# Kernel optimization log

Hardware: AMD Instinct MI355X
Metric: run time of the kernel (lower is better)

Reference implementation:

```python
import jax, jax.numpy as jnp
import numpy as np

B, S, HID = 2, 2048, 2048
H, HKV, HD = 16, 8, 128
INPUT_CHUNK, RET_CHUNK = 256, 64
NUM_CHUNKS = S // INPUT_CHUNK - 1          # 7 retrieval chunks
INPUT_START = NUM_CHUNKS * RET_CHUNK       # 448
KV_LEN = S + INPUT_START                   # 2496
SCALE = HD ** -0.5


def _document_id():
    d = np.zeros(KV_LEN, np.int32)
    d[INPUT_START:] = -1
    for i in range(NUM_CHUNKS):            # retrieval chunks get ids 1..NUM_CHUNKS
        d[RET_CHUNK * i: RET_CHUNK * (i + 1)] = i + 1
    for i in range(1, NUM_CHUNKS + 1):     # input chunk i (i>=1) gets id i
        d[INPUT_START + INPUT_CHUNK * i: INPUT_START + INPUT_CHUNK * (i + 1)] = i
    return d


def _causal_retrieval_mask():
    d = _document_id()
    q = np.arange(S)[:, None]
    kv = np.arange(KV_LEN)[None, :]
    causal = (q + INPUT_START >= kv) & (kv > INPUT_START)
    docm = (d[q + INPUT_START] == d[kv]) & (kv < INPUT_START)
    return jnp.asarray(causal | docm)      # [S, KV_LEN] bool


_MASK = _causal_retrieval_mask()


def rotate_half(x):
    x1, x2 = jnp.split(x, 2, axis=-1)
    return jnp.concatenate([-x2, x1], axis=-1)


def setup_inputs() -> dict:
    key = jax.random.key(0)
    ks = jax.random.split(key, 8)
    hidden_states = jax.random.normal(ks[0], (B, S, HID), jnp.float32)
    # standard llama RoPE tables
    pos = jnp.arange(S, dtype=jnp.float32)
    inv = 1.0 / (10000.0 ** (jnp.arange(0, HD, 2, dtype=jnp.float32) / HD))
    f = pos[:, None] * inv[None, :]
    emb = jnp.concatenate([f, f], axis=-1)
    cos = jnp.broadcast_to(jnp.cos(emb), (B, S, HD)).astype(jnp.float32)
    sin = jnp.broadcast_to(jnp.sin(emb), (B, S, HD)).astype(jnp.float32)
    retrieval_key_states = jax.random.normal(ks[1], (B * NUM_CHUNKS, HKV, RET_CHUNK, HD), jnp.float32)
    retrieval_value_states = jax.random.normal(ks[2], (B * NUM_CHUNKS, HKV, RET_CHUNK, HD), jnp.float32)
    s = 0.02
    Wq = jax.random.normal(ks[3], (HID, H * HD), jnp.float32) * s
    Wk = jax.random.normal(ks[4], (HID, HKV * HD), jnp.float32) * s
    Wv = jax.random.normal(ks[5], (HID, HKV * HD), jnp.float32) * s
    Wo = jax.random.normal(ks[6], (H * HD, HID), jnp.float32) * s
    return {"hidden_states": hidden_states, "cos": cos, "sin": sin,
            "retrieval_key_states": retrieval_key_states,
            "retrieval_value_states": retrieval_value_states,
            "Wq": Wq, "Wk": Wk, "Wv": Wv, "Wo": Wo}


def reference(hidden_states, cos, sin, retrieval_key_states, retrieval_value_states, Wq, Wk, Wv, Wo):
    b = hidden_states.shape[0]
    # QKV projections (bias=False), -> [b, h, s, d]
    q = (hidden_states @ Wq).reshape(b, S, H, HD).transpose(0, 2, 1, 3)
    k = (hidden_states @ Wk).reshape(b, S, HKV, HD).transpose(0, 2, 1, 3)
    v = (hidden_states @ Wv).reshape(b, S, HKV, HD).transpose(0, 2, 1, 3)
    # RoPE (cos/sin unsqueezed over heads)
    c = cos[:, None]
    sn = sin[:, None]
    q = q * c + rotate_half(q) * sn
    k = k * c + rotate_half(k) * sn
    # retrieval KV: (b*nc, hkv, rc, d) -> (b, hkv, nc*rc, d)
    rk = retrieval_key_states.reshape(b, NUM_CHUNKS, HKV, RET_CHUNK, HD).transpose(0, 2, 1, 3, 4).reshape(b, HKV, NUM_CHUNKS * RET_CHUNK, HD)
    rv = retrieval_value_states.reshape(b, NUM_CHUNKS, HKV, RET_CHUNK, HD).transpose(0, 2, 1, 3, 4).reshape(b, HKV, NUM_CHUNKS * RET_CHUNK, HD)
    k_all = jnp.concatenate([rk, k], axis=2)     # [b, hkv, KV_LEN, d]
    v_all = jnp.concatenate([rv, v], axis=2)
    # GQA: repeat kv heads
    g = H // HKV
    k_all = jnp.repeat(k_all, g, axis=1)
    v_all = jnp.repeat(v_all, g, axis=1)
    scores = jnp.einsum('bhqd,bhkd->bhqk', q, k_all) * SCALE
    neg = jnp.finfo(scores.dtype).min
    scores = jnp.where(_MASK[None, None], scores, neg)
    probs = jax.nn.softmax(scores, axis=-1)
    # fully-masked rows (q_idx=0) -> 0 output, matching flex_attention semantics
    probs = jnp.where(_MASK[None, None], probs, 0.0)
    attn = jnp.einsum('bhqk,bhkd->bhqd', probs, v_all)   # [b, H, S, HD]
    # NOTE: source reshapes (b, H, S, HD) directly to (b, S, H*HD) with NO transpose
    attn = attn.reshape(b, S, H * HD)
    return attn @ Wo
```

## Files before the change

### kernel.cpp

```cpp
#include <hip/hip_runtime.h>

#define B_ 2
#define S_ 2048
#define HID_ 2048
#define H_ 16
#define HKV_ 8
#define HD_ 128
#define NCH_ 7
#define RET_ 64
#define IST_ 448
#define KVL_ 2496
#define SCALE_ 0.08838834764831845f
#define SC2_ (0.08838834764831845f * 1.44269504088896340f)
#define MCAP_ 16.0f

typedef __attribute__((ext_vector_type(8))) short short8;
typedef __attribute__((ext_vector_type(4))) short short4v;
typedef __attribute__((ext_vector_type(4))) float f32x4;

static __device__ __forceinline__ unsigned short f2bf(float f) {
    unsigned u = __float_as_uint(f);
    unsigned r = (u + 0x7fffu + ((u >> 16) & 1u)) >> 16;
    return (unsigned short)r;
}
static __device__ __forceinline__ float bf2f(unsigned short x) {
    return __uint_as_float(((unsigned)x) << 16);
}

#define GLL16(gp, lp) __builtin_amdgcn_global_load_lds( \
    (__attribute__((address_space(1))) void*)(void*)(gp), \
    (__attribute__((address_space(3))) void*)(void*)(lp), 16, 0, 0)

__global__ __launch_bounds__(256) void prep_in_kernel(const float* __restrict__ hidden,
                                                      const float* __restrict__ Wq,
                                                      const float* __restrict__ Wk,
                                                      const float* __restrict__ Wv,
                                                      const float* __restrict__ Wo,
                                                      unsigned short* __restrict__ hb,
                                                      unsigned short* __restrict__ wqkvT,
                                                      unsigned short* __restrict__ woT) {
    const int bid = blockIdx.x;
    const int tid = threadIdx.x;
    if (bid < 8192) {
        int i = bid * 256 + tid;
        float4 v = ((const float4*)hidden)[i];
        ushort4 o;
        o.x = f2bf(v.x); o.y = f2bf(v.y); o.z = f2bf(v.z); o.w = f2bf(v.w);
        ((ushort4*)hb)[i] = o;
    } else {
        __shared__ float t[32][33];
        const int tbid = bid - 8192;
        const int z = tbid >> 12;
        const int xy = tbid & 4095;
        const int k0 = (xy & 63) << 5, n0 = (xy >> 6) << 5;
        const float* W;
        unsigned short* WT;
        int N;
        if (z == 0)      { W = Wq; WT = wqkvT;                        N = 2048; }
        else if (z == 1) { W = Wk; WT = wqkvT + (size_t)2048 * 2048;  N = 1024; }
        else if (z == 2) { W = Wv; WT = wqkvT + (size_t)3072 * 2048;  N = 1024; }
        else             { W = Wo; WT = woT;                          N = 2048; }
        if (n0 >= N) return;
        const int tx = tid & 31, ty = tid >> 5;
#pragma unroll
        for (int i = 0; i < 4; i++)
            t[ty + i * 8][tx] = W[(size_t)(k0 + ty + i * 8) * N + n0 + tx];
        __syncthreads();
#pragma unroll
        for (int i = 0; i < 4; i++)
            WT[(size_t)(n0 + ty + i * 8) * 2048 + k0 + tx] = f2bf(t[tx][ty + i * 8]);
    }
}

template <int BN, typename OT>
__global__ __launch_bounds__(512, 2) void gemm256(const unsigned short* __restrict__ A,
                                                  const unsigned short* __restrict__ BT,
                                                  OT* __restrict__ C,
                                                  int M, int N, int K) {
    constexpr int NJ = BN / 64;
    __shared__ short As[2][16384];
    __shared__ short Bs[2][BN * 64];
    const int tid = threadIdx.x;
    const int wid = tid >> 6, lane = tid & 63;
    const int lq = lane & 15, lk = lane >> 4;
    const int wm = wid >> 2, wn = wid & 3;
    const int bm = blockIdx.x, bn = blockIdx.y;

    const int rowin = tid >> 3;
    const int koff = (((tid & 7) ^ (rowin & 7)) << 3);
    const size_t abase = (size_t)(bm * 256 + rowin) * K;
    const size_t bbase = (size_t)(bn * BN + rowin) * K;
    const int ldst = wid * 512;

    f32x4 acc[8][NJ] = {};

    auto stageA = [&](int buf, int k0, int r) {
        GLL16(A + abase + (size_t)(r * 64) * K + k0 + koff, &As[buf][r * 4096 + ldst]);
    };
    auto stageB = [&](int buf, int k0, int r) {
        GLL16(BT + bbase + (size_t)(r * 64) * K + k0 + koff, &Bs[buf][r * 4096 + ldst]);
    };
    auto stageAll = [&](int buf, int k0) {
#pragma unroll
        for (int r = 0; r < 4; r++) stageA(buf, k0, r);
#pragma unroll
        for (int r = 0; r < NJ; r++) stageB(buf, k0, r);
    };

    const int nk = K >> 6;
    stageAll(0, 0);
    __syncthreads();
    for (int t = 0; t < nk; t++) {
        const int cur = t & 1;
        const bool pf = (t + 1 < nk);
        const int nk0 = (t + 1) << 6;
        short8 bf[2][NJ];
#pragma unroll
        for (int j = 0; j < NJ; j++)
#pragma unroll
            for (int kk = 0; kk < 2; kk++) {
                const int row = wn * (BN / 4) + j * 16 + lq;
                bf[kk][j] = *(const short8*)&Bs[cur][row * 64 +
                                                     (((kk * 4 + lk) ^ (lq & 7)) << 3)];
            }
#pragma unroll
        for (int p = 0; p < 4; p++) {
            if (pf) {
                stageA(cur ^ 1, nk0, p);
                if (p < NJ) stageB(cur ^ 1, nk0, p);
            }
            short8 af0[2], af1[2];
#pragma unroll
            for (int kk = 0; kk < 2; kk++) {
                const int r0 = wm * 128 + (2 * p) * 16 + lq;
                const int r1 = wm * 128 + (2 * p + 1) * 16 + lq;
                af0[kk] = *(const short8*)&As[cur][r0 * 64 +
                                                   (((kk * 4 + lk) ^ (lq & 7)) << 3)];
                af1[kk] = *(const short8*)&As[cur][r1 * 64 +
                                                   (((kk * 4 + lk) ^ (lq & 7)) << 3)];
            }
            __builtin_amdgcn_s_setprio(1);
#pragma unroll
            for (int j = 0; j < NJ; j++)
#pragma unroll
                for (int kk = 0; kk < 2; kk++) {
                    acc[2 * p][j] =
                        __builtin_amdgcn_mfma_f32_16x16x32_bf16(bf[kk][j], af0[kk], acc[2 * p][j], 0, 0, 0);
                    acc[2 * p + 1][j] =
                        __builtin_amdgcn_mfma_f32_16x16x32_bf16(bf[kk][j], af1[kk], acc[2 * p + 1][j], 0, 0, 0);
                }
            __builtin_amdgcn_s_setprio(0);
        }
        __syncthreads();
    }
#pragma unroll
    for (int i = 0; i < 8; i++) {
        const size_t row = (size_t)(bm * 256 + wm * 128 + i * 16 + lq);
#pragma unroll
        for (int j = 0; j < NJ; j++) {
            const size_t col = (size_t)(bn * BN + wn * (BN / 4) + j * 16 + lk * 4);
            if constexpr (sizeof(OT) == 2) {
                ushort4 u;
                u.x = f2bf(acc[i][j][0]);
                u.y = f2bf(acc[i][j][1]);
                u.z = f2bf(acc[i][j][2]);
                u.w = f2bf(acc[i][j][3]);
                *(ushort4*)&C[row * N + col] = u;
            } else {
                *(f32x4*)&C[row * N + col] = acc[i][j];
            }
        }
    }
}

__global__ __launch_bounds__(256) void prep_kv_kernel(const unsigned short* __restrict__ qkvraw,
                                                      const float* __restrict__ cosb,
                                                      const float* __restrict__ sinb,
                                                      const float* __restrict__ rk,
                                                      const float* __restrict__ rv,
                                                      unsigned short* __restrict__ kall,
                                                      unsigned short* __restrict__ vt) {
    const int bid = blockIdx.x;
    const int tid = threadIdx.x;
    if (bid < 2048) {
        unsigned u = (unsigned)bid * 256 + tid;
        int d0 = (u & 15) << 2;
        int hk = (u >> 4) & 7;
        unsigned bs = u >> 7;
        int b = (int)(bs >> 11), s = (int)(bs & 2047);
        size_t base = (size_t)bs * 4096 + 2048 + hk * 128 + d0;
        short4v x1 = *(const short4v*)(qkvraw + base);
        short4v x2 = *(const short4v*)(qkvraw + base + 64);
        float4 c1 = *(const float4*)(cosb + (size_t)s * 128 + d0);
        float4 s1 = *(const float4*)(sinb + (size_t)s * 128 + d0);
        float4 c2 = *(const float4*)(cosb + (size_t)s * 128 + d0 + 64);
        float4 s2 = *(const float4*)(sinb + (size_t)s * 128 + d0 + 64);
        const float cc1[4] = {c1.x, c1.y, c1.z, c1.w}, ss1[4] = {s1.x, s1.y, s1.z, s1.w};
        const float cc2[4] = {c2.x, c2.y, c2.z, c2.w}, ss2[4] = {s2.x, s2.y, s2.z, s2.w};
        size_t o = ((size_t)(b * HKV_ + hk) * KVL_ + IST_ + s) * HD_ + d0;
        ushort4 w1, w2;
        unsigned short r1[4], r2[4];
#pragma unroll
        for (int e = 0; e < 4; e++) {
            float a = bf2f((unsigned short)x1[e]);
            float bb = bf2f((unsigned short)x2[e]);
            r1[e] = f2bf(a * cc1[e] - bb * ss1[e]);
            r2[e] = f2bf(bb * cc2[e] + a * ss2[e]);
        }
        w1.x = r1[0]; w1.y = r1[1]; w1.z = r1[2]; w1.w = r1[3];
        w2.x = r2[0]; w2.y = r2[1]; w2.z = r2[2]; w2.w = r2[3];
        *(ushort4*)(kall + o) = w1;
        *(ushort4*)(kall + o + 64) = w2;
    } else if (bid < 2944) {
        unsigned u = (unsigned)(bid - 2048) * 256 + tid;
        int d0 = (u & 31) << 2;
        int r = (u >> 5) & 63;
        int hk = (u >> 11) & 7;
        int bc = (int)(u >> 14);
        int b = bc / NCH_, ch = bc % NCH_;
        float4 v = *(const float4*)(rk + (((size_t)(bc * HKV_ + hk) * RET_ + r) * HD_ + d0));
        ushort4 w;
        w.x = f2bf(v.x); w.y = f2bf(v.y); w.z = f2bf(v.z); w.w = f2bf(v.w);
        *(ushort4*)(kall + ((size_t)(b * HKV_ + hk) * KVL_ + ch * RET_ + r) * HD_ + d0) = w;
    } else {
        const int vbid = bid - 2944;
        const int tx = tid & 31, ty = tid >> 5;
        if (vbid < 4096) {
            __shared__ unsigned short t[32][33];
            const int d0 = (vbid & 3) << 5, s0 = ((vbid >> 2) & 63) << 5;
            const int bh = vbid >> 8;
            const int b = bh >> 3, hk = bh & 7;
#pragma unroll
            for (int i = 0; i < 4; i++)
                t[ty + i * 8][tx] =
                    qkvraw[(size_t)(b * S_ + s0 + ty + i * 8) * 4096 + 3072 + hk * 128 + d0 + tx];
            __syncthreads();
#pragma unroll
            for (int i = 0; i < 4; i++)
                vt[((size_t)(b * HKV_ + hk) * HD_ + d0 + ty + i * 8) * KVL_ + IST_ + s0 + tx] =
                    t[tx][ty + i * 8];
        } else {
            __shared__ float tf[32][33];
            const int bid2 = vbid - 4096;
            const int d0 = (bid2 & 3) << 5;
            const int r0 = ((bid2 >> 2) & 1) << 5;
            const int z = bid2 >> 3;
            const int bc = z >> 3, hk = z & 7;
            const int b = bc / NCH_, ch = bc % NCH_;
#pragma unroll
            for (int i = 0; i < 4; i++)
                tf[ty + i * 8][tx] =
                    rv[((size_t)(bc * HKV_ + hk) * RET_ + r0 + ty + i * 8) * HD_ + d0 + tx];
            __syncthreads();
#pragma unroll
            for (int i = 0; i < 4; i++)
                vt[((size_t)(b * HKV_ + hk) * HD_ + d0 + ty + i * 8) * KVL_ + ch * RET_ + r0 + tx] =
                    f2bf(tf[tx][ty + i * 8]);
        }
    }
}

__global__ __launch_bounds__(1024) void attn_kernel(const unsigned short* __restrict__ qkvraw,
                                                    const unsigned short* __restrict__ kall,
                                                    const unsigned short* __restrict__ vt,
                                                    const float* __restrict__ cosb,
                                                    const float* __restrict__ sinb,
                                                    unsigned short* __restrict__ attnb) {
    __shared__ short Ks[2][16384];
    __shared__ short Vs[2][16384];
    __shared__ short Ps[16][1024];
    const int tid = threadIdx.x;
    const int wid = tid >> 6, lane = tid & 63;
    const int lq = lane & 15, lk = lane >> 4;
    const int pairi = blockIdx.x;
    const int h = blockIdx.y, b = blockIdx.z, hk = h >> 1;
    const unsigned short* kbase = kall + (size_t)(b * HKV_ + hk) * KVL_ * HD_;
    const unsigned short* vbase = vt + (size_t)(b * HKV_ + hk) * HD_ * KVL_;

    int row_[2], xc_[2];
#pragma unroll
    for (int p = 0; p < 2; p++) {
        int o = p * 16384 + tid * 16;
        row_[p] = o >> 8;
        xc_[p] = (tid & 15) ^ (row_[p] & 7);
    }
    short* psw = &Ps[wid][0];

    const int qlo = pairi * 128, qhi = (15 - pairi) * 128;
    const int wgrp = wid >> 3;
    const int qb0 = wgrp ? qhi : qlo;
    const int qbw = qb0 + (wid & 7) * 16;
    const int doc_lo = qlo >> 8;
    const int doc_hi = qhi >> 8;
    const int kvA = RET_ * ((doc_lo >= 1 ? doc_lo : 1) - 1);
    const int kvB = RET_ * (doc_hi - 1);
    const int nt = 17 - pairi;

    const unsigned short* qrp = qkvraw + ((size_t)(b * S_) + qbw + lq) * 4096 + h * 128;
    short8 qr[4];
#pragma unroll
    for (int d = 0; d < 4; d++) qr[d] = *(const short8*)(qrp + d * 32 + lk * 8);
    const float* cosp = cosb + (size_t)(qbw + lq) * 128 + lk * 8;
    const float* sinp = sinb + (size_t)(qbw + lq) * 128 + lk * 8;
    short8 qf[4];
#pragma unroll
    for (int d = 0; d < 4; d++) {
        float4 c0 = *(const float4*)(cosp + d * 32);
        float4 c1 = *(const float4*)(cosp + d * 32 + 4);
        float4 s0 = *(const float4*)(sinp + d * 32);
        float4 s1 = *(const float4*)(sinp + d * 32 + 4);
        const float cc[8] = {c0.x, c0.y, c0.z, c0.w, c1.x, c1.y, c1.z, c1.w};
        const float ss[8] = {s0.x, s0.y, s0.z, s0.w, s1.x, s1.y, s1.z, s1.w};
        const int od = d ^ 2;
        const float sg = (d < 2) ? -1.f : 1.f;
#pragma unroll
        for (int e = 0; e < 8; e++) {
            float x = bf2f((unsigned short)qr[d][e]);
            float y = bf2f((unsigned short)qr[od][e]);
            qf[d][e] = (short)f2bf(fmaf(sg * y, ss[e], x * cc[e]));
        }
    }

    f32x4 o[8] = {};
    float lsump = 0.f;

    auto stage = [&](int buf, int kv0) {
#pragma unroll
        for (int p = 0; p < 2; p++) {
            GLL16(kbase + (size_t)(kv0 + row_[p]) * HD_ + xc_[p] * 8,
                  &Ks[buf][p * 8192 + wid * 512]);
            GLL16(vbase + (size_t)row_[p] * KVL_ + kv0 + xc_[p] * 8,
                  &Vs[buf][p * 8192 + wid * 512]);
        }
    };
    auto stage_ret = [&](int buf) {
#pragma unroll
        for (int p = 0; p < 2; p++) {
            int kr = row_[p];
            int ks = (kr < 64) ? kvA + kr : kvB + (kr - 64);
            GLL16(kbase + (size_t)ks * HD_ + xc_[p] * 8, &Ks[buf][p * 8192 + wid * 512]);
            int vc = (xc_[p] < 8) ? kvA + xc_[p] * 8 : kvB + (xc_[p] - 8) * 8;
            GLL16(vbase + (size_t)row_[p] * KVL_ + vc, &Vs[buf][p * 8192 + wid * 512]);
        }
    };
    auto smpv = [&](f32x4* sa4, int hb8, const char* vb) {
#pragma unroll
        for (int j2 = 0; j2 < 4; j2++) {
            float p0 = __builtin_amdgcn_exp2f(fmaf(sa4[j2][0], SC2_, -MCAP_));
            float p1 = __builtin_amdgcn_exp2f(fmaf(sa4[j2][1], SC2_, -MCAP_));
            float p2 = __builtin_amdgcn_exp2f(fmaf(sa4[j2][2], SC2_, -MCAP_));
            float p3 = __builtin_amdgcn_exp2f(fmaf(sa4[j2][3], SC2_, -MCAP_));
            lsump += (p0 + p1) + (p2 + p3);
            uint2 w;
            asm("v_cvt_pk_bf16_f32 %0, %1, %2" : "=v"(w.x) : "v"(p0), "v"(p1));
            asm("v_cvt_pk_bf16_f32 %0, %1, %2" : "=v"(w.y) : "v"(p2), "v"(p3));
            *(uint2*)((char*)psw + (lq * 128 + ((j2 * 32 + lk * 8) ^ ((lq & 7) << 4)))) = w;
        }
        __builtin_amdgcn_s_setprio(1);
#pragma unroll
        for (int ks = 0; ks < 2; ks++) {
            short8 pa = *(const short8*)((const char*)psw +
                                         (lq * 128 + (((ks * 4 + lk) ^ (lq & 7)) << 4)));
#pragma unroll
            for (int db = 0; db < 8; db++) {
                short8 vf = *(const short8*)(vb + ((db * 16 + lq) * 256 +
                                                   (((hb8 + ks * 4 + lk) ^ (lq & 7)) << 4)));
                o[db] = __builtin_amdgcn_mfma_f32_16x16x32_bf16(pa, vf, o[db], 0, 0, 0);
            }
        }
        __builtin_amdgcn_s_setprio(0);
    };

    stage_ret(0);
    asm volatile("s_waitcnt vmcnt(0)" ::: "memory");
    __syncthreads();
    int cur = 0;
    for (int t = 0; t < nt; t++) {
        if (t + 1 < nt) stage(cur ^ 1, IST_ + t * 128);
        const char* kb = (const char*)&Ks[cur][0];
        const char* vb = (const char*)&Vs[cur][0];
        if (t == 0) {
            const bool retact = (wgrp == 1) || (doc_lo >= 1);
            if (retact) {
                const int hh = wgrp;
                f32x4 sa[4] = {};
                __builtin_amdgcn_s_setprio(1);
#pragma unroll
                for (int d = 0; d < 4; d++)
#pragma unroll
                    for (int j2 = 0; j2 < 4; j2++) {
                        short8 kf = *(const short8*)(kb + (((hh * 4 + j2) * 16 + lq) * 256 +
                                                           (((d * 4 + lk) ^ (lq & 7)) << 4)));
                        sa[j2] = __builtin_amdgcn_mfma_f32_16x16x32_bf16(kf, qf[d], sa[j2], 0, 0, 0);
                    }
                __builtin_amdgcn_s_setprio(0);
                smpv(sa, hh * 8, vb);
            }
        } else {
            const int kv0 = IST_ + (t - 1) * 128;
            const bool active = kv0 <= qbw + 15 + IST_;
            if (active) {
                const bool act2 = (kv0 + 64 <= qbw + 15 + IST_);
                f32x4 sa[8] = {};
                __builtin_amdgcn_s_setprio(1);
#pragma unroll
                for (int d = 0; d < 4; d++)
#pragma unroll
                    for (int j = 0; j < 4; j++) {
                        short8 kf = *(const short8*)(kb + ((j * 16 + lq) * 256 +
                                                           (((d * 4 + lk) ^ (lq & 7)) << 4)));
                        sa[j] = __builtin_amdgcn_mfma_f32_16x16x32_bf16(kf, qf[d], sa[j], 0, 0, 0);
                    }
                if (act2) {
#pragma unroll
                    for (int d = 0; d < 4; d++)
#pragma unroll
                        for (int j = 4; j < 8; j++) {
                            short8 kf = *(const short8*)(kb + ((j * 16 + lq) * 256 +
                                                               (((d * 4 + lk) ^ (lq & 7)) << 4)));
                            sa[j] = __builtin_amdgcn_mfma_f32_16x16x32_bf16(kf, qf[d], sa[j], 0, 0, 0);
                        }
                }
                __builtin_amdgcn_s_setprio(0);
                const int qg = qbw + lq;
                if (kv0 == IST_ || kv0 + 63 > qbw + IST_) {
#pragma unroll
                    for (int j = 0; j < 4; j++)
#pragma unroll
                        for (int r = 0; r < 4; r++) {
                            int kg = kv0 + j * 16 + lk * 4 + r;
                            if (!(kg > IST_ && kg <= qg + IST_)) sa[j][r] = -3e38f;
                        }
                }
                if (act2 && kv0 + 127 > qbw + IST_) {
#pragma unroll
                    for (int j = 4; j < 8; j++)
#pragma unroll
                        for (int r = 0; r < 4; r++) {
                            int kg = kv0 + j * 16 + lk * 4 + r;
                            if (kg > qg + IST_) sa[j][r] = -3e38f;
                        }
                }
                smpv(&sa[0], 0, vb);
                if (act2) smpv(&sa[4], 8, vb);
            }
        }
        if (t + 1 < nt) asm volatile("s_waitcnt vmcnt(0)" ::: "memory");
        __syncthreads();
        cur ^= 1;
    }

    float ls = lsump;
    ls += __shfl_xor(ls, 16);
    ls += __shfl_xor(ls, 32);
    float inv[4];
#pragma unroll
    for (int r = 0; r < 4; r++) {
        float v = __shfl(ls, lk * 4 + r);
        inv[r] = v > 0.f ? 1.f / v : 0.f;
    }
#pragma unroll
    for (int db = 0; db < 8; db++)
#pragma unroll
        for (int r = 0; r < 4; r++) {
            int qg = qbw + lk * 4 + r;
            size_t row = (size_t)b * 2048 + h * 128 + (qg >> 4);
            size_t col = (size_t)(qg & 15) * 128 + db * 16 + lq;
            attnb[row * 2048 + col] = f2bf(o[db][r] * inv[r]);
        }
}

extern "C" void kernel_launch(void* const* d_in, const int* in_sizes, int n_in,
                              void* d_out, int out_size, void* d_ws, size_t ws_size,
                              hipStream_t stream) {
    const float* hidden = (const float*)d_in[0];
    const float* cosb = (const float*)d_in[1];
    const float* sinb = (const float*)d_in[2];
    const float* rk = (const float*)d_in[3];
    const float* rv = (const float*)d_in[4];
    const float* Wq = (const float*)d_in[5];
    const float* Wk = (const float*)d_in[6];
    const float* Wv = (const float*)d_in[7];
    const float* Wo = (const float*)d_in[8];
    float* out = (float*)d_out;

    char* ws = (char*)d_ws;
    unsigned short* hb     = (unsigned short*)(ws + 0);
    unsigned short* wqkvT  = (unsigned short*)(ws + 16777216);
    unsigned short* woT    = (unsigned short*)(ws + 33554432);
    unsigned short* qkvraw = (unsigned short*)(ws + 41943040);
    unsigned short* kallb  = (unsigned short*)(ws + 92274688);
    unsigned short* vtb    = (unsigned short*)(ws + 102498304);
    unsigned short* attnb  = (unsigned short*)(ws + 112721920);

    prep_in_kernel<<<24576, 256, 0, stream>>>(hidden, Wq, Wk, Wv, Wo, hb, wqkvT, woT);

    gemm256<256, unsigned short><<<dim3(16, 16), 512, 0, stream>>>(hb, wqkvT, qkvraw, 4096, 4096, 2048);

    prep_kv_kernel<<<7936, 256, 0, stream>>>(qkvraw, cosb, sinb, rk, rv, kallb, vtb);

    attn_kernel<<<dim3(8, 16, 2), 1024, 0, stream>>>(qkvraw, kallb, vtb, cosb, sinb, attnb);

    gemm256<128, float><<<dim3(16, 16), 512, 0, stream>>>(attnb, woT, out, 4096, 2048, 2048);
}
```

Measured before the change: 211.4 us.

## Split high-q causal KV tiles across both wave groups after low block finishes

Once the low query block's causal range has been covered, the first wave group stores its output and switches to the high query block. From then on both wave groups take alternate KV tiles for the high block, staging two tiles per step. Their partial outputs and row sums are merged through shared memory at the end, and the merge relies on a fixed softmax max cap. The aim is to remove the load imbalance where group 0 sat idle while group 1 worked through the long causal tail. The cost is extra syncs, a shared-memory combine and fewer prefetch overlaps in the paired phase.

```diff
diff --git a/kernel.cpp b/kernel.cpp
--- a/kernel.cpp
+++ b/kernel.cpp
@@ -288,38 +288,46 @@
 
     const int qlo = pairi * 128, qhi = (15 - pairi) * 128;
     const int wgrp = wid >> 3;
+    const int w8 = wid & 7;
     const int qb0 = wgrp ? qhi : qlo;
-    const int qbw = qb0 + (wid & 7) * 16;
+    const int qbw = qb0 + w8 * 16;
+    const int qbw2 = qhi + w8 * 16;
     const int doc_lo = qlo >> 8;
     const int doc_hi = qhi >> 8;
     const int kvA = RET_ * ((doc_lo >= 1 ? doc_lo : 1) - 1);
     const int kvB = RET_ * (doc_hi - 1);
-    const int nt = 17 - pairi;
-
-    const unsigned short* qrp = qkvraw + ((size_t)(b * S_) + qbw + lq) * 4096 + h * 128;
-    short8 qr[4];
-#pragma unroll
-    for (int d = 0; d < 4; d++) qr[d] = *(const short8*)(qrp + d * 32 + lk * 8);
-    const float* cosp = cosb + (size_t)(qbw + lq) * 128 + lk * 8;
-    const float* sinp = sinb + (size_t)(qbw + lq) * 128 + lk * 8;
+    const int t1end = pairi + 1;
+    const int nt1 = pairi + 2;
+    const int Tmax = 16 - pairi;
+    const int npair = (Tmax - t1end + 1) >> 1;
+
     short8 qf[4];
-#pragma unroll
-    for (int d = 0; d < 4; d++) {
-        float4 c0 = *(const float4*)(cosp + d * 32);
-        float4 c1 = *(const float4*)(cosp + d * 32 + 4);
-        float4 s0 = *(const float4*)(sinp + d * 32);
-        float4 s1 = *(const float4*)(sinp + d * 32 + 4);
-        const float cc[8] = {c0.x, c0.y, c0.z, c0.w, c1.x, c1.y, c1.z, c1.w};
-        const float ss[8] = {s0.x, s0.y, s0.z, s0.w, s1.x, s1.y, s1.z, s1.w};
-        const int od = d ^ 2;
-        const float sg = (d < 2) ? -1.f : 1.f;
-#pragma unroll
-        for (int e = 0; e < 8; e++) {
-            float x = bf2f((unsigned short)qr[d][e]);
-            float y = bf2f((unsigned short)qr[od][e]);
-            qf[d][e] = (short)f2bf(fmaf(sg * y, ss[e], x * cc[e]));
-        }
-    }
+    auto load_q = [&](int myqb) {
+        const unsigned short* qrp = qkvraw + ((size_t)(b * S_) + myqb + lq) * 4096 + h * 128;
+        short8 qr[4];
+#pragma unroll
+        for (int d = 0; d < 4; d++) qr[d] = *(const short8*)(qrp + d * 32 + lk * 8);
+        const float* cosp = cosb + (size_t)(myqb + lq) * 128 + lk * 8;
+        const float* sinp = sinb + (size_t)(myqb + lq) * 128 + lk * 8;
+#pragma unroll
+        for (int d = 0; d < 4; d++) {
+            float4 c0 = *(const float4*)(cosp + d * 32);
+            float4 c1 = *(const float4*)(cosp + d * 32 + 4);
+            float4 s0 = *(const float4*)(sinp + d * 32);
+            float4 s1 = *(const float4*)(sinp + d * 32 + 4);
+            const float cc[8] = {c0.x, c0.y, c0.z, c0.w, c1.x, c1.y, c1.z, c1.w};
+            const float ss[8] = {s0.x, s0.y, s0.z, s0.w, s1.x, s1.y, s1.z, s1.w};
+            const int od = d ^ 2;
+            const float sg = (d < 2) ? -1.f : 1.f;
+#pragma unroll
+            for (int e = 0; e < 8; e++) {
+                float x = bf2f((unsigned short)qr[d][e]);
+                float y = bf2f((unsigned short)qr[od][e]);
+                qf[d][e] = (short)f2bf(fmaf(sg * y, ss[e], x * cc[e]));
+            }
+        }
+    };
+    load_q(qbw);
 
     f32x4 o[8] = {};
     float lsump = 0.f;
@@ -370,13 +378,58 @@
         }
         __builtin_amdgcn_s_setprio(0);
     };
+    auto causal_tile = [&](const char* kb, const char* vb, int kv0, int myqb) {
+        const bool act2 = (kv0 + 64 <= myqb + 15 + IST_);
+        f32x4 sa[8] = {};
+        __builtin_amdgcn_s_setprio(1);
+#pragma unroll
+        for (int d = 0; d < 4; d++)
+#pragma unroll
+            for (int j = 0; j < 4; j++) {
+                short8 kf = *(const short8*)(kb + ((j * 16 + lq) * 256 +
+                                                   (((d * 4 + lk) ^ (lq & 7)) << 4)));
+                sa[j] = __builtin_amdgcn_mfma_f32_16x16x32_bf16(kf, qf[d], sa[j], 0, 0, 0);
+            }
+        if (act2) {
+#pragma unroll
+            for (int d = 0; d < 4; d++)
+#pragma unroll
+                for (int j = 4; j < 8; j++) {
+                    short8 kf = *(const short8*)(kb + ((j * 16 + lq) * 256 +
+                                                       (((d * 4 + lk) ^ (lq & 7)) << 4)));
+                    sa[j] = __builtin_amdgcn_mfma_f32_16x16x32_bf16(kf, qf[d], sa[j], 0, 0, 0);
+                }
+        }
+        __builtin_amdgcn_s_setprio(0);
+        const int qg = myqb + lq;
+        if (kv0 == IST_ || kv0 + 63 > myqb + IST_) {
+#pragma unroll
+            for (int j = 0; j < 4; j++)
+#pragma unroll
+                for (int r = 0; r < 4; r++) {
+                    int kg = kv0 + j * 16 + lk * 4 + r;
+                    if (!(kg > IST_ && kg <= qg + IST_)) sa[j][r] = -3e38f;
+                }
+        }
+        if (act2 && kv0 + 127 > myqb + IST_) {
+#pragma unroll
+            for (int j = 4; j < 8; j++)
+#pragma unroll
+                for (int r = 0; r < 4; r++) {
+                    int kg = kv0 + j * 16 + lk * 4 + r;
+                    if (kg > qg + IST_) sa[j][r] = -3e38f;
+                }
+        }
+        smpv(&sa[0], 0, vb);
+        if (act2) smpv(&sa[4], 8, vb);
+    };
 
     stage_ret(0);
     asm volatile("s_waitcnt vmcnt(0)" ::: "memory");
     __syncthreads();
     int cur = 0;
-    for (int t = 0; t < nt; t++) {
-        if (t + 1 < nt) stage(cur ^ 1, IST_ + t * 128);
+    for (int t = 0; t < nt1; t++) {
+        if (t + 1 < nt1) stage(cur ^ 1, IST_ + t * 128);
         const char* kb = (const char*)&Ks[cur][0];
         const char* vb = (const char*)&Vs[cur][0];
         if (t == 0) {
@@ -398,76 +451,86 @@
             }
         } else {
             const int kv0 = IST_ + (t - 1) * 128;
-            const bool active = kv0 <= qbw + 15 + IST_;
-            if (active) {
-                const bool act2 = (kv0 + 64 <= qbw + 15 + IST_);
-                f32x4 sa[8] = {};
-                __builtin_amdgcn_s_setprio(1);
-#pragma unroll
-                for (int d = 0; d < 4; d++)
-#pragma unroll
-                    for (int j = 0; j < 4; j++) {
-                        short8 kf = *(const short8*)(kb + ((j * 16 + lq) * 256 +
-                                                           (((d * 4 + lk) ^ (lq & 7)) << 4)));
-                        sa[j] = __builtin_amdgcn_mfma_f32_16x16x32_bf16(kf, qf[d], sa[j], 0, 0, 0);
-                    }
-                if (act2) {
-#pragma unroll
-                    for (int d = 0; d < 4; d++)
-#pragma unroll
-                        for (int j = 4; j < 8; j++) {
-                            short8 kf = *(const short8*)(kb + ((j * 16 + lq) * 256 +
-                                                               (((d * 4 + lk) ^ (lq & 7)) << 4)));
-                            sa[j] = __builtin_amdgcn_mfma_f32_16x16x32_bf16(kf, qf[d], sa[j], 0, 0, 0);
-                        }
-                }
-                __builtin_amdgcn_s_setprio(0);
-                const int qg = qbw + lq;
-                if (kv0 == IST_ || kv0 + 63 > qbw + IST_) {
-#pragma unroll
-                    for (int j = 0; j < 4; j++)
-#pragma unroll
-                        for (int r = 0; r < 4; r++) {
-                            int kg = kv0 + j * 16 + lk * 4 + r;
-                            if (!(kg > IST_ && kg <= qg + IST_)) sa[j][r] = -3e38f;
-                        }
-                }
-                if (act2 && kv0 + 127 > qbw + IST_) {
-#pragma unroll
-                    for (int j = 4; j < 8; j++)
-#pragma unroll
-                        for (int r = 0; r < 4; r++) {
-                            int kg = kv0 + j * 16 + lk * 4 + r;
-                            if (kg > qg + IST_) sa[j][r] = -3e38f;
-                        }
-                }
-                smpv(&sa[0], 0, vb);
-                if (act2) smpv(&sa[4], 8, vb);
-            }
-        }
-        if (t + 1 < nt) asm volatile("s_waitcnt vmcnt(0)" ::: "memory");
+            if (kv0 <= qbw + 15 + IST_) causal_tile(kb, vb, kv0, qbw);
+        }
+        if (t + 1 < nt1) asm volatile("s_waitcnt vmcnt(0)" ::: "memory");
         __syncthreads();
         cur ^= 1;
     }
 
-    float ls = lsump;
-    ls += __shfl_xor(ls, 16);
-    ls += __shfl_xor(ls, 32);
-    float inv[4];
-#pragma unroll
-    for (int r = 0; r < 4; r++) {
-        float v = __shfl(ls, lk * 4 + r);
-        inv[r] = v > 0.f ? 1.f / v : 0.f;
-    }
-#pragma unroll
-    for (int db = 0; db < 8; db++)
+    if (wgrp == 0) {
+        float ls = lsump;
+        ls += __shfl_xor(ls, 16);
+        ls += __shfl_xor(ls, 32);
+        float inv[4];
 #pragma unroll
         for (int r = 0; r < 4; r++) {
-            int qg = qbw + lk * 4 + r;
-            size_t row = (size_t)b * 2048 + h * 128 + (qg >> 4);
-            size_t col = (size_t)(qg & 15) * 128 + db * 16 + lq;
-            attnb[row * 2048 + col] = f2bf(o[db][r] * inv[r]);
-        }
+            float v = __shfl(ls, lk * 4 + r);
+            inv[r] = v > 0.f ? 1.f / v : 0.f;
+        }
+#pragma unroll
+        for (int db = 0; db < 8; db++) {
+#pragma unroll
+            for (int r = 0; r < 4; r++) {
+                int qg = qbw + lk * 4 + r;
+                size_t row = (size_t)b * 2048 + h * 128 + (qg >> 4);
+                size_t col = (size_t)(qg & 15) * 128 + db * 16 + lq;
+                attnb[row * 2048 + col] = f2bf(o[db][r] * inv[r]);
+            }
+            o[db] = (f32x4){0.f, 0.f, 0.f, 0.f};
+        }
+        lsump = 0.f;
+        load_q(qbw2);
+    }
+
+    for (int s = 0; s < npair; s++) {
+        const int TA = t1end + 1 + 2 * s;
+        const int TB = TA + 1;
+        stage(0, IST_ + (TA - 1) * 128);
+        if (TB <= Tmax) stage(1, IST_ + (TB - 1) * 128);
+        asm volatile("s_waitcnt vmcnt(0)" ::: "memory");
+        __syncthreads();
+        const int Tg = TA + wgrp;
+        if (Tg <= Tmax) {
+            causal_tile((const char*)&Ks[wgrp][0], (const char*)&Vs[wgrp][0],
+                        IST_ + (Tg - 1) * 128, qbw2);
+        }
+        __syncthreads();
+    }
+
+    float* cmbO = (float*)&Ks[0][0];
+    float* cmbL = (float*)&Vs[0][0];
+    if (wgrp == 0) {
+#pragma unroll
+        for (int db = 0; db < 8; db++)
+            *(f32x4*)&cmbO[((w8 * 8 + db) * 64 + lane) * 4] = o[db];
+        cmbL[w8 * 64 + lane] = lsump;
+    }
+    __syncthreads();
+    if (wgrp == 1) {
+#pragma unroll
+        for (int db = 0; db < 8; db++)
+            o[db] += *(const f32x4*)&cmbO[((w8 * 8 + db) * 64 + lane) * 4];
+        lsump += cmbL[w8 * 64 + lane];
+        float ls = lsump;
+        ls += __shfl_xor(ls, 16);
+        ls += __shfl_xor(ls, 32);
+        float inv[4];
+#pragma unroll
+        for (int r = 0; r < 4; r++) {
+            float v = __shfl(ls, lk * 4 + r);
+            inv[r] = v > 0.f ? 1.f / v : 0.f;
+        }
+#pragma unroll
+        for (int db = 0; db < 8; db++)
+#pragma unroll
+            for (int r = 0; r < 4; r++) {
+                int qg = qbw + lk * 4 + r;
+                size_t row = (size_t)b * 2048 + h * 128 + (qg >> 4);
+                size_t col = (size_t)(qg & 15) * 128 + db * 16 + lq;
+                attnb[row * 2048 + col] = f2bf(o[db][r] * inv[r]);
+            }
+    }
 }
 
 extern "C" void kernel_launch(void* const* d_in, const int* in_sizes, int n_in,
```

Measured after the change: 217.2 us. +2.7%, slower.
